# Kernel optimization log

Measured on AMD Instinct MI355X. Metric: run time of the kernel, lower is better.

## Reference

```python
import jax, jax.numpy as jnp
import numpy as np

C_IN = 256
C_RED = max(4, C_IN // 4)  # 64


def setup_inputs() -> dict:
    key = jax.random.key(0)
    k1, k2, k3, k4, k5 = jax.random.split(key, 5)
    B, C, H, W = 4, C_IN, 64, 64
    x = jax.random.normal(k1, (B, C, H, W), dtype=jnp.float32)
    # 1x1 convs (no bias) are just channel matmuls: weight shape (out_ch, in_ch)
    s_in = 1.0 / np.sqrt(C)
    s_red = 1.0 / np.sqrt(C_RED)
    Wq = jax.random.normal(k2, (C_RED, C), dtype=jnp.float32) * s_in
    Wk = jax.random.normal(k3, (C_RED, C), dtype=jnp.float32) * s_in
    Wv = jax.random.normal(k4, (C_RED, C), dtype=jnp.float32) * s_in
    Wp = jax.random.normal(k5, (C, C_RED), dtype=jnp.float32) * s_red
    return {"x": x, "Wq": Wq, "Wk": Wk, "Wv": Wv, "Wp": Wp}


def reference(x, Wq, Wk, Wv, Wp):
    B, C, H, W = x.shape
    N = H * W
    xf = x.reshape(B, C, N)                       # (B, C, N)
    q = jnp.einsum('rc,bcn->bnr', Wq, xf)         # (B, N, c_red)
    k = jnp.einsum('rc,bcn->brn', Wk, xf)         # (B, c_red, N)
    v = jnp.einsum('rc,bcn->bnr', Wv, xf)         # (B, N, c_red)
    scale = 1.0 / jnp.sqrt(jnp.float32(k.shape[1]))
    attn = jnp.einsum('bnr,brm->bnm', q, k) * scale   # (B, N, N)
    attn = jax.nn.softmax(attn, axis=-1)
    out = jnp.einsum('bnm,bmr->brn', attn, v)     # (B, c_red, N)
    out = jnp.einsum('cr,brn->bcn', Wp, out)      # (B, C, N)
    return out.reshape(B, C, H, W) + x
```

## Files before the change

kernel.cpp:

```cpp
#include <hip/hip_runtime.h>
#include <hip/hip_bf16.h>

#define CIN 256
#define CRED 64
#define NB 4
#define NN 4096

typedef float v4f __attribute__((ext_vector_type(4)));
typedef short v8s __attribute__((ext_vector_type(8)));
typedef unsigned short u16;
typedef u16 u16x4 __attribute__((ext_vector_type(4)));
typedef u16 u16x8 __attribute__((ext_vector_type(8)));
typedef unsigned int u32;

#define LOG2E 1.4426950408889634f

__device__ __forceinline__ u16 f2bf(float f) {
    union { float f; u32 u; } v; v.f = f;
    u32 r = (v.u + 0x7FFFu + ((v.u >> 16) & 1u)) >> 16;
    return (u16)r;
}
__device__ __forceinline__ float bf2f(u16 s) {
    union { u32 u; float f; } v; v.u = ((u32)s) << 16;
    return v.f;
}
__device__ __forceinline__ u32 pkbf(float a, float b) {
    float2 f; f.x = a; f.y = b;
    __hip_bfloat162 h = __float22bfloat162_rn(f);
    union { __hip_bfloat162 h; u32 u; } c; c.h = h;
    return c.u;
}
__device__ __forceinline__ v4f mfma16(v8s a, v8s b, v4f c) {
    return __builtin_amdgcn_mfma_f32_16x16x32_bf16(a, b, c, 0, 0, 0);
}
__device__ __forceinline__ float fexp2(float x) {
#if __has_builtin(__builtin_amdgcn_exp2f)
    return __builtin_amdgcn_exp2f(x);
#else
    return exp2f(x);
#endif
}

__global__ __launch_bounds__(256) void k_wconv(const float* __restrict__ Wq,
                                               const float* __restrict__ Wk,
                                               const float* __restrict__ Wv,
                                               u16* __restrict__ Wb) {
    int t = threadIdx.x;
    int idx = (blockIdx.x * 256 + t) * 4;
    int row = idx >> 8;
    int mat = row >> 6, r = row & 63, col = idx & 255;
    const float* src = (mat == 0) ? Wq : (mat == 1) ? Wk : Wv;
    float4 v = *(const float4*)&src[r * 256 + col];
    float s = (mat == 0) ? (0.125f * LOG2E) : 1.0f;
    u16x4 o;
    o[0] = f2bf(v.x * s); o[1] = f2bf(v.y * s);
    o[2] = f2bf(v.z * s); o[3] = f2bf(v.w * s);
    *(u16x4*)&Wb[idx] = o;
}

__global__ __launch_bounds__(256) void k_qkvm(const float* __restrict__ x,
                                              const u16* __restrict__ Wb,
                                              u16* __restrict__ Q, u16* __restrict__ K,
                                              u16* __restrict__ V) {
    __shared__ __align__(16) u16 Xl[1056 * 8];
    int t = threadIdx.x;
    int wv = t >> 6, lane = t & 63, c15 = lane & 15, quad = lane >> 4;
    int n0g = blockIdx.x * 32;
    int b = n0g >> 12, nb = n0g & 4095;
    const float* xb = x + ((size_t)b << 20);

    {
        int cb = t >> 3, n4 = (t & 7) * 4;
        const float* px = xb + (size_t)(cb * 8) * 4096 + nb + n4;
        float4 f[8];
#pragma unroll
        for (int j = 0; j < 8; ++j)
            f[j] = *(const float4*)&px[(size_t)j * 4096];
#pragma unroll
        for (int i = 0; i < 4; ++i) {
            union { u16x8 v; u32 w[4]; } pk;
            pk.w[0] = pkbf(((const float*)&f[0])[i], ((const float*)&f[1])[i]);
            pk.w[1] = pkbf(((const float*)&f[2])[i], ((const float*)&f[3])[i]);
            pk.w[2] = pkbf(((const float*)&f[4])[i], ((const float*)&f[5])[i]);
            pk.w[3] = pkbf(((const float*)&f[6])[i], ((const float*)&f[7])[i]);
            *(u16x8*)&Xl[(size_t)(cb * 33 + n4 + i) * 8] = pk.v;
        }
    }
    __syncthreads();

    v8s Af[2][8];
#pragma unroll
    for (int nt = 0; nt < 2; ++nt)
#pragma unroll
        for (int kc = 0; kc < 8; ++kc)
            Af[nt][kc] = *(const v8s*)&Xl[(size_t)((kc * 4 + quad) * 33 + nt * 16 + c15) * 8];

#pragma unroll
    for (int rti = 0; rti < 3; ++rti) {
        int rt = wv * 3 + rti;
        const u16* wrow = Wb + (size_t)(rt * 16 + c15) * 256 + quad * 8;
        v8s Bf[8];
#pragma unroll
        for (int kc = 0; kc < 8; ++kc) Bf[kc] = *(const v8s*)&wrow[kc * 32];
#pragma unroll
        for (int nt = 0; nt < 2; ++nt) {
            v4f acc = {0.f, 0.f, 0.f, 0.f};
#pragma unroll
            for (int kc = 0; kc < 8; ++kc)
                acc = mfma16(Af[nt][kc], Bf[kc], acc);
            if (rt < 8) {
                u16* base = (rt < 4) ? Q : K;
                u16* dst = base + ((size_t)b << 18)
                         + (size_t)(nb + nt * 16 + quad * 4) * 64
                         + (rt & 3) * 16 + c15;
#pragma unroll
                for (int g = 0; g < 4; ++g) dst[g * 64] = f2bf(acc[g]);
            } else {
                int hi2 = ((nb + nt * 16) >> 4) & 3;
                size_t base = ((size_t)b * 64 + (rt - 8) * 16 + c15) * 4096
                            + (size_t)((nb + nt * 16) & ~63) + hi2;
#pragma unroll
                for (int g = 0; g < 4; ++g)
                    V[base + (quad * 4 + g) * 4] = f2bf(acc[g]);
            }
        }
    }
}

__global__ __launch_bounds__(256, 3) void k_flash(const u16* __restrict__ Q,
                                                  const u16* __restrict__ K,
                                                  const u16* __restrict__ V,
                                                  u16* __restrict__ OP,
                                                  float* __restrict__ Lb,
                                                  int sh) {
    __shared__ __align__(16) u16 KV[2][2][4096];
    __shared__ __align__(16) u16 Pl[4][32][72];
    int t = threadIdx.x;
    int p = blockIdx.x & ((1u << sh) - 1);
    int tile = blockIdx.x >> sh;
    int b = tile >> 5;
    int n0 = (tile & 31) * 128;
    int wv = t >> 6;
    int lane = t & 63;
    int c15 = lane & 15;
    int quad = lane >> 4;
    int nw = n0 + wv * 32;
    const u16* Qb = Q + ((size_t)b << 18);
    const u16* Kb = K + ((size_t)b << 18);
    const u16* Vb = V + ((size_t)b << 18);

    v8s Qa[2][2];
#pragma unroll
    for (int rg = 0; rg < 2; ++rg)
#pragma unroll
        for (int c2 = 0; c2 < 2; ++c2)
            Qa[rg][c2] = *(const v8s*)&Qb[(size_t)(nw + rg * 16 + c15) * 64 + c2 * 32 + quad * 8];

    union { u16x8 u; v8s s; } on;
#pragma unroll
    for (int j = 0; j < 8; ++j) on.u[j] = 0x3F80;

    v4f O[2][4];
    v4f Lacc[2];
#pragma unroll
    for (int rg = 0; rg < 2; ++rg) {
#pragma unroll
        for (int g = 0; g < 4; ++g) {
            Lacc[rg][g] = 0.f;
#pragma unroll
            for (int cg = 0; cg < 4; ++cg) O[rg][cg][g] = 0.f;
        }
    }

    int mlen = NN >> sh;
    int m0 = p * mlen;
    int iters = mlen >> 6;

    int lrow = lane >> 3;
    int cs16 = (((lane & 7) ^ lrow) << 3);
    const u16* gK = Kb + ((size_t)(wv * 16 + lrow) << 6) + cs16;
    const u16* gV = Vb + ((size_t)(wv * 16 + lrow) << 12) + cs16;

    auto stage = [&](int buf, int mt) {
#pragma unroll
        for (int i = 0; i < 2; ++i) {
            __builtin_amdgcn_global_load_lds(
                (const __attribute__((address_space(1))) void*)(gK + ((size_t)(mt + i * 8) << 6)),
                (__attribute__((address_space(3))) void*)&KV[buf][0][(wv * 2 + i) << 9],
                16, 0, 0);
            __builtin_amdgcn_global_load_lds(
                (const __attribute__((address_space(1))) void*)(gV + ((size_t)i << 15) + mt),
                (__attribute__((address_space(3))) void*)&KV[buf][1][(wv * 2 + i) << 9],
                16, 0, 0);
        }
    };

    int swz = (c15 & 7) << 4;
    int col0 = (quad << 4) ^ swz;
    int col1 = col0 ^ 64;
    int rbase = c15 << 7;

    stage(0, m0);
    __syncthreads();

    for (int it = 0; it < iters; ++it) {
        int cur = it & 1;
        if (it + 1 < iters) stage(cur ^ 1, m0 + (it + 1) * 64);
        const char* KB = (const char*)&KV[cur][0][0];
        const char* VB = (const char*)&KV[cur][1][0];

        v4f S[2][4];
#pragma unroll
        for (int rg = 0; rg < 2; ++rg)
#pragma unroll
            for (int s = 0; s < 4; ++s)
#pragma unroll
                for (int g = 0; g < 4; ++g) S[rg][s][g] = 0.f;

        __builtin_amdgcn_s_setprio(1);
#pragma unroll
        for (int s = 0; s < 4; ++s) {
            v8s kb0 = *(const v8s*)(KB + rbase + s * 2048 + col0);
            v8s kb1 = *(const v8s*)(KB + rbase + s * 2048 + col1);
            S[0][s] = mfma16(Qa[0][0], kb0, S[0][s]);
            S[1][s] = mfma16(Qa[1][0], kb0, S[1][s]);
            S[0][s] = mfma16(Qa[0][1], kb1, S[0][s]);
            S[1][s] = mfma16(Qa[1][1], kb1, S[1][s]);
        }
        __builtin_amdgcn_s_setprio(0);

#pragma unroll
        for (int rg = 0; rg < 2; ++rg) {
#pragma unroll
            for (int g = 0; g < 4; ++g) {
                float e0 = fexp2(S[rg][0][g]);
                float e1 = fexp2(S[rg][1][g]);
                float e2 = fexp2(S[rg][2][g]);
                float e3 = fexp2(S[rg][3][g]);
                union { u16x4 v; u32 w[2]; } p2;
                p2.w[0] = pkbf(e0, e1);
                p2.w[1] = pkbf(e2, e3);
                *(u16x4*)&Pl[wv][rg * 16 + quad * 4 + g][c15 * 4] = p2.v;
            }
        }

        v8s Pa[2][2];
#pragma unroll
        for (int rg = 0; rg < 2; ++rg)
#pragma unroll
            for (int c2 = 0; c2 < 2; ++c2)
                Pa[rg][c2] = *(const v8s*)&Pl[wv][rg * 16 + c15][c2 * 32 + quad * 8];

        __builtin_amdgcn_s_setprio(1);
#pragma unroll
        for (int cg = 0; cg < 4; ++cg) {
            v8s vb0 = *(const v8s*)(VB + (cg << 11) + rbase + col0);
            v8s vb1 = *(const v8s*)(VB + (cg << 11) + rbase + col1);
            O[0][cg] = mfma16(Pa[0][0], vb0, O[0][cg]);
            O[1][cg] = mfma16(Pa[1][0], vb0, O[1][cg]);
            O[0][cg] = mfma16(Pa[0][1], vb1, O[0][cg]);
            O[1][cg] = mfma16(Pa[1][1], vb1, O[1][cg]);
        }
        Lacc[0] = mfma16(Pa[0][0], on.s, Lacc[0]);
        Lacc[0] = mfma16(Pa[0][1], on.s, Lacc[0]);
        Lacc[1] = mfma16(Pa[1][0], on.s, Lacc[1]);
        Lacc[1] = mfma16(Pa[1][1], on.s, Lacc[1]);
        __builtin_amdgcn_s_setprio(0);
        __syncthreads();
    }

    u16* OPp = OP + (size_t)p * (NB * NN * 64) + (size_t)b * NN * 64;
#pragma unroll
    for (int rg = 0; rg < 2; ++rg)
#pragma unroll
        for (int cg = 0; cg < 4; ++cg)
#pragma unroll
            for (int g = 0; g < 4; ++g) {
                int n = nw + rg * 16 + quad * 4 + g;
                OPp[(size_t)n * 64 + cg * 16 + c15] = f2bf(O[rg][cg][g]);
            }
    if (c15 == 0) {
        float* Lp = Lb + (size_t)p * (NB * NN) + (size_t)b * NN;
#pragma unroll
        for (int rg = 0; rg < 2; ++rg)
#pragma unroll
            for (int g = 0; g < 4; ++g) {
                int n = nw + rg * 16 + quad * 4 + g;
                Lp[n] = Lacc[rg][g];
            }
    }
}

#define OMP 72
template <int NSP>
__global__ __launch_bounds__(256) void k_proj(const u16* __restrict__ OP,
                                              const float* __restrict__ Lb,
                                              const float* __restrict__ Wp,
                                              const float* __restrict__ x,
                                              float* __restrict__ out) {
    __shared__ __align__(16) u16 Om[32 * OMP];
    int t = threadIdx.x;
    int b = blockIdx.x >> 7;
    int n0 = (blockIdx.x & 127) * 32;

    {
        int n_l = t >> 3, r0 = (t & 7) * 8;
        size_t nidx = (size_t)b * NN + n0 + n_l;
        float o[8] = {0.f, 0.f, 0.f, 0.f, 0.f, 0.f, 0.f, 0.f};
        float l = 0.f;
#pragma unroll
        for (int p = 0; p < NSP; ++p) {
            u16x8 u = *(const u16x8*)&OP[((size_t)p * (NB * NN) + nidx) * 64 + r0];
#pragma unroll
            for (int j = 0; j < 8; ++j) o[j] += bf2f(u[j]);
            l += Lb[(size_t)p * (NB * NN) + nidx];
        }
        float inv = 1.0f / l;
        union { u16x8 v; u32 w[4]; } p2;
        p2.w[0] = pkbf(o[0] * inv, o[1] * inv);
        p2.w[1] = pkbf(o[2] * inv, o[3] * inv);
        p2.w[2] = pkbf(o[4] * inv, o[5] * inv);
        p2.w[3] = pkbf(o[6] * inv, o[7] * inv);
        *(u16x8*)&Om[n_l * OMP + r0] = p2.v;
    }
    __syncthreads();

    int lane = t & 63, wvv = t >> 6, c15 = lane & 15, quad = lane >> 4;
    v8s Bf[2][2];
#pragma unroll
    for (int nt = 0; nt < 2; ++nt) {
        Bf[nt][0] = *(const v8s*)&Om[(nt * 16 + c15) * OMP + quad * 8];
        Bf[nt][1] = *(const v8s*)&Om[(nt * 16 + c15) * OMP + 32 + quad * 8];
    }
#pragma unroll
    for (int ct0 = 0; ct0 < 4; ++ct0) {
        int ct = wvv * 4 + ct0;
        const float* wrow = Wp + (size_t)(ct * 16 + c15) * 64 + quad * 8;
        float4 wa = *(const float4*)&wrow[0];
        float4 wb = *(const float4*)&wrow[4];
        float4 wc = *(const float4*)&wrow[32];
        float4 wd = *(const float4*)&wrow[36];
        union { v8s s; u32 w[4]; } A0, A1;
        A0.w[0] = pkbf(wa.x, wa.y); A0.w[1] = pkbf(wa.z, wa.w);
        A0.w[2] = pkbf(wb.x, wb.y); A0.w[3] = pkbf(wb.z, wb.w);
        A1.w[0] = pkbf(wc.x, wc.y); A1.w[1] = pkbf(wc.z, wc.w);
        A1.w[2] = pkbf(wd.x, wd.y); A1.w[3] = pkbf(wd.z, wd.w);
#pragma unroll
        for (int nt = 0; nt < 2; ++nt) {
            v4f acc = {0.f, 0.f, 0.f, 0.f};
            acc = mfma16(A0.s, Bf[nt][0], acc);
            acc = mfma16(A1.s, Bf[nt][1], acc);
            size_t base = ((size_t)(b * 256 + ct * 16 + quad * 4)) * 4096 + n0 + nt * 16 + c15;
#pragma unroll
            for (int g = 0; g < 4; ++g)
                out[base + (size_t)g * 4096] = acc[g] + x[base + (size_t)g * 4096];
        }
    }
}

extern "C" void kernel_launch(void* const* d_in, const int* in_sizes, int n_in,
                              void* d_out, int out_size, void* d_ws, size_t ws_size,
                              hipStream_t stream) {
    const float* x  = (const float*)d_in[0];
    const float* Wq = (const float*)d_in[1];
    const float* Wk = (const float*)d_in[2];
    const float* Wv = (const float*)d_in[3];
    const float* Wp = (const float*)d_in[4];
    float* out = (float*)d_out;
    char* ws = (char*)d_ws;

    const int nsp = 4;
    const int sh = 2;

    u16* Wb  = (u16*)(ws);
    u16* Q   = (u16*)(ws + 262144);
    u16* K   = (u16*)(ws + 262144 + 2097152);
    u16* V   = (u16*)(ws + 262144 + 2 * 2097152);
    u16* OP  = (u16*)(ws + 262144 + 3 * 2097152);
    float* Lbuf = (float*)(ws + 262144 + (size_t)(3 + nsp) * 2097152);

    k_wconv<<<48, 256, 0, stream>>>(Wq, Wk, Wv, Wb);
    k_qkvm<<<512, 256, 0, stream>>>(x, Wb, Q, K, V);
    k_flash<<<NB * 32 * nsp, 256, 0, stream>>>(Q, K, V, OP, Lbuf, sh);
    k_proj<4><<<NB * 128, 256, 0, stream>>>(OP, Lbuf, Wp, x, out);
}
```

Measured before the change: 117.8 us.

## Keep softmax probabilities in registers by transposing QK MFMA and permuting V layout

```diff
diff --git a/kernel.cpp b/kernel.cpp
--- a/kernel.cpp
+++ b/kernel.cpp
@@ -118,23 +118,24 @@
             } else {
                 int hi2 = ((nb + nt * 16) >> 4) & 3;
                 size_t base = ((size_t)b * 64 + (rt - 8) * 16 + c15) * 4096
-                            + (size_t)((nb + nt * 16) & ~63) + hi2;
-#pragma unroll
-                for (int g = 0; g < 4; ++g)
-                    V[base + (quad * 4 + g) * 4] = f2bf(acc[g]);
+                            + (size_t)((nb + nt * 16) & ~63)
+                            + (hi2 >> 1) * 32 + (hi2 & 1) * 4 + quad * 8;
+                union { u16x4 v; u32 w[2]; } pv;
+                pv.w[0] = pkbf(acc[0], acc[1]);
+                pv.w[1] = pkbf(acc[2], acc[3]);
+                *(u16x4*)&V[base] = pv.v;
             }
         }
     }
 }
 
-__global__ __launch_bounds__(256, 3) void k_flash(const u16* __restrict__ Q,
+__global__ __launch_bounds__(256, 2) void k_flash(const u16* __restrict__ Q,
                                                   const u16* __restrict__ K,
                                                   const u16* __restrict__ V,
                                                   u16* __restrict__ OP,
                                                   float* __restrict__ Lb,
                                                   int sh) {
     __shared__ __align__(16) u16 KV[2][2][4096];
-    __shared__ __align__(16) u16 Pl[4][32][72];
     int t = threadIdx.x;
     int p = blockIdx.x & ((1u << sh) - 1);
     int tile = blockIdx.x >> sh;
@@ -222,34 +223,26 @@
         for (int s = 0; s < 4; ++s) {
             v8s kb0 = *(const v8s*)(KB + rbase + s * 2048 + col0);
             v8s kb1 = *(const v8s*)(KB + rbase + s * 2048 + col1);
-            S[0][s] = mfma16(Qa[0][0], kb0, S[0][s]);
-            S[1][s] = mfma16(Qa[1][0], kb0, S[1][s]);
-            S[0][s] = mfma16(Qa[0][1], kb1, S[0][s]);
-            S[1][s] = mfma16(Qa[1][1], kb1, S[1][s]);
+            S[0][s] = mfma16(kb0, Qa[0][0], S[0][s]);
+            S[1][s] = mfma16(kb0, Qa[1][0], S[1][s]);
+            S[0][s] = mfma16(kb1, Qa[0][1], S[0][s]);
+            S[1][s] = mfma16(kb1, Qa[1][1], S[1][s]);
         }
         __builtin_amdgcn_s_setprio(0);
 
-#pragma unroll
-        for (int rg = 0; rg < 2; ++rg) {
-#pragma unroll
-            for (int g = 0; g < 4; ++g) {
-                float e0 = fexp2(S[rg][0][g]);
-                float e1 = fexp2(S[rg][1][g]);
-                float e2 = fexp2(S[rg][2][g]);
-                float e3 = fexp2(S[rg][3][g]);
-                union { u16x4 v; u32 w[2]; } p2;
-                p2.w[0] = pkbf(e0, e1);
-                p2.w[1] = pkbf(e2, e3);
-                *(u16x4*)&Pl[wv][rg * 16 + quad * 4 + g][c15 * 4] = p2.v;
+        v8s Pa[2][2];
+#pragma unroll
+        for (int rg = 0; rg < 2; ++rg)
+#pragma unroll
+            for (int c2 = 0; c2 < 2; ++c2) {
+                int s0 = c2 * 2, s1 = c2 * 2 + 1;
+                union { v8s s; u32 w[4]; } pk;
+                pk.w[0] = pkbf(fexp2(S[rg][s0][0]), fexp2(S[rg][s0][1]));
+                pk.w[1] = pkbf(fexp2(S[rg][s0][2]), fexp2(S[rg][s0][3]));
+                pk.w[2] = pkbf(fexp2(S[rg][s1][0]), fexp2(S[rg][s1][1]));
+                pk.w[3] = pkbf(fexp2(S[rg][s1][2]), fexp2(S[rg][s1][3]));
+                Pa[rg][c2] = pk.s;
             }
-        }
-
-        v8s Pa[2][2];
-#pragma unroll
-        for (int rg = 0; rg < 2; ++rg)
-#pragma unroll
-            for (int c2 = 0; c2 < 2; ++c2)
-                Pa[rg][c2] = *(const v8s*)&Pl[wv][rg * 16 + c15][c2 * 32 + quad * 8];
 
         __builtin_amdgcn_s_setprio(1);
 #pragma unroll
```

New measurement: 114.4 us. 1.03x faster.
